# Kernel tuning notes

Hardware: AMD Instinct MI355X
Metric: run time of the kernel (lower is better)

## Reference

```python
import jax, jax.numpy as jnp
import numpy as np
import math

MAX_L = 3
N_RBF = 8
CUTOFF = 5.5
P_CUT = 6
ZS = (1, 6, 7, 8)
N_NODES = 10000
N_EDGES = 60000
N_EMB = 3  # n_atom_basis; edge channels = N_EMB**2 = 9


def _lxlylz_list(max_l):
    lst = []
    for l in range(max_l + 1):
        for lx in range(l, -1, -1):
            for ly in range(l - lx, -1, -1):
                lst.append((lx, ly, l - lx - ly))
    return lst

LXLYLZ = _lxlylz_list(MAX_L)            # 20 monomial exponent triples
IDX = {v: i for i, v in enumerate(LXLYLZ)}
L_OF = np.array([sum(v) for v in LXLYLZ], dtype=np.int32)
LX = jnp.array([v[0] for v in LXLYLZ])
LY = jnp.array([v[1] for v in LXLYLZ])
LZ = jnp.array([v[2] for v in LXLYLZ])
L_OF_J = jnp.array(L_OF)
ZS_J = jnp.array(ZS)


def _multinom(v):
    l = sum(v)
    return math.factorial(l) // (math.factorial(v[0]) * math.factorial(v[1]) * math.factorial(v[2]))


def _splits(l):
    return [v for v in LXLYLZ if sum(v) == l]


def _nu2_terms():
    # B2_l = sum_{|lvec|=l} multinom(lvec) * A_lvec^2  (contraction of (r1.r2)^l)
    out = []
    for l in range(1, MAX_L + 1):
        vs = _splits(l)
        idx = jnp.array([IDX[v] for v in vs])
        pref = jnp.array([float(_multinom(v)) for v in vs], dtype=jnp.float32)
        out.append((idx, idx, pref))
    return out


def _nu3_terms():
    # invariants from (r1.r2)^e12 (r1.r3)^e13 (r2.r3)^e23, all e>=1, vector degrees <= MAX_L
    combos = [(a, b, c) for a in range(1, MAX_L + 1) for b in range(1, MAX_L + 1)
              for c in range(1, MAX_L + 1) if a + b <= MAX_L and a + c <= MAX_L and b + c <= MAX_L]
    out = []
    for (e12, e13, e23) in combos:
        coef = {}
        for va in _splits(e12):
            for vb in _splits(e13):
                for vc in _splits(e23):
                    v1 = (va[0] + vb[0], va[1] + vb[1], va[2] + vb[2])
                    v2 = (va[0] + vc[0], va[1] + vc[1], va[2] + vc[2])
                    v3 = (vb[0] + vc[0], vb[1] + vc[1], vb[2] + vc[2])
                    key = (v1, v2, v3)
                    coef[key] = coef.get(key, 0.0) + float(_multinom(va) * _multinom(vb) * _multinom(vc))
        keys = list(coef.keys())
        i1 = jnp.array([IDX[k[0]] for k in keys])
        i2 = jnp.array([IDX[k[1]] for k in keys])
        i3 = jnp.array([IDX[k[2]] for k in keys])
        pref = jnp.array([coef[k] for k in keys], dtype=jnp.float32)
        out.append((i1, i2, i3, pref))
    return out

NU2_TERMS = _nu2_terms()
NU3_TERMS = _nu3_terms()


def setup_inputs() -> dict:
    key = jax.random.key(0)
    k1, k2, k3, k4, k5 = jax.random.split(key, 5)
    positions = jax.random.uniform(k1, (N_NODES, 3), dtype=jnp.float32) * 4.0  # box so most r < cutoff
    atomic_numbers = ZS_J[jax.random.randint(k2, (N_NODES,), 0, len(ZS))]
    edge_index = jax.random.randint(k3, (2, N_EDGES), 0, N_NODES)
    shifts = jnp.zeros((N_EDGES, 3), jnp.float32)
    embedding_weight = jax.random.normal(k4, (len(ZS), N_EMB), jnp.float32) / np.sqrt(len(ZS))
    radial_weight = jax.random.normal(k5, (MAX_L + 1, N_RBF, N_RBF), jnp.float32) / np.sqrt(N_RBF)
    return {"positions": positions, "shifts": shifts, "embedding_weight": embedding_weight,
            "radial_weight": radial_weight, "atomic_numbers": atomic_numbers, "edge_index": edge_index}


def reference(positions, shifts, embedding_weight, radial_weight, atomic_numbers, edge_index):
    # node one-hot + embedding
    onehot = (atomic_numbers[:, None] == ZS_J[None, :]).astype(positions.dtype)
    emb = onehot @ embedding_weight                                   # [N, n_emb]
    snd, rcv = edge_index[0], edge_index[1]
    E = snd.shape[0]
    # directed edge encoding: outer product of endpoint embeddings -> [E, n_emb^2]
    enc = (emb[snd][:, :, None] * emb[rcv][:, None, :]).reshape(E, -1)
    # edge vectors / lengths (normalized)
    vec = positions[rcv] - positions[snd] + shifts
    length = jnp.maximum(jnp.linalg.norm(vec, axis=-1, keepdims=True), 1e-9)  # [E,1]
    unit = vec / length
    # Bessel RBF * polynomial cutoff
    n = jnp.arange(1, N_RBF + 1, dtype=positions.dtype)
    rbf = jnp.sqrt(2.0 / CUTOFF) * jnp.sin(n * jnp.pi * length / CUTOFF) / length  # [E,R]
    x = length / CUTOFF
    p = float(P_CUT)
    fc = (1.0 - 0.5 * (p + 1) * (p + 2) * x ** P_CUT + p * (p + 2) * x ** (P_CUT + 1)
          - 0.5 * p * (p + 1) * x ** (P_CUT + 2)) * (x < 1.0)
    radial = rbf * fc                                                  # [E,R]
    # angular monomials x^lx y^ly z^lz
    pw = unit[:, :, None] ** jnp.arange(MAX_L + 1)                     # [E,3,L+1]
    ang = pw[:, 0, LX] * pw[:, 1, LY] * pw[:, 2, LZ]                   # [E,A=20]
    # triple outer product -> per-edge attribute tensor [E,R,A,C]
    edge_attr = jnp.einsum('er,ea,ec->erac', radial, ang, enc)
    # shared per-l radial linear transform
    Wa = radial_weight[L_OF_J]                                         # [A,R,R]
    edge_attr = jnp.einsum('ars,erac->esac', Wa, edge_attr)
    # scatter-sum to receiver nodes -> A basis
    A = jax.ops.segment_sum(edge_attr, rcv, num_segments=positions.shape[0])  # [N,R,A,C]
    # symmetrizer: invariant B basis up to nu=3
    feats = [A[:, :, 0, :]]                                            # nu=1: A_{000}
    for i1, i2, pref in NU2_TERMS:
        feats.append(jnp.einsum('t,nrtc->nrc', pref, A[:, :, i1, :] * A[:, :, i2, :]))
    for i1, i2, i3, pref in NU3_TERMS:
        feats.append(jnp.einsum('t,nrtc->nrc', pref, A[:, :, i1, :] * A[:, :, i2, :] * A[:, :, i3, :]))
    return jnp.stack(feats, axis=2)                                    # [N, R, n_B=8, C]
```

## Files before the change

kernel.cpp:

```cpp
#include <hip/hip_runtime.h>

constexpr int NRBF = 8;
constexpr int NA   = 20;
constexpr int NC   = 9;
constexpr int EDW  = 64;
constexpr int CAP  = 64;
constexpr int STG  = 16;

__constant__ int cLX[NA] = {0,1,0,0,2,1,1,0,0,0,3,2,2,1,1,1,0,0,0,0};
__constant__ int cLY[NA] = {0,0,1,0,0,1,0,2,1,0,0,1,0,2,1,0,3,2,1,0};
__constant__ int cLZ[NA] = {0,0,0,1,0,0,1,0,1,2,0,0,1,0,1,2,0,1,2,3};
__constant__ int cLOF[NA]= {0,1,1,1,2,2,2,2,2,2,3,3,3,3,3,3,3,3,3,3};
constexpr int kLOF[NA]  = {0,1,1,1,2,2,2,2,2,2,3,3,3,3,3,3,3,3,3,3};

__device__ __forceinline__ int zmap(int z) {
    return z == 1 ? 0 : (z == 6 ? 1 : (z == 7 ? 2 : 3));
}

struct Nu3Tbl {
    int n;
    unsigned char i1[200], i2[200], i3[200], cb[200];
    float pref[200];
};
constexpr int idx_of(int lx, int ly, int lz) {
    int l = lx + ly + lz;
    int base = (l == 0) ? 0 : ((l == 1) ? 1 : ((l == 2) ? 4 : 10));
    int d = l - lx;
    return base + d * (d + 1) / 2 + (d - ly);
}
constexpr int factc(int k) { return k <= 1 ? 1 : k * factc(k - 1); }
constexpr float multinom(int lx, int ly, int lz) {
    return (float)(factc(lx + ly + lz) / (factc(lx) * factc(ly) * factc(lz)));
}
constexpr Nu3Tbl make_nu3() {
    Nu3Tbl t{};
    const int combos[4][3] = {{1,1,1},{1,1,2},{1,2,1},{2,1,1}};
    for (int q = 0; q < 4; ++q) {
        int e12 = combos[q][0], e13 = combos[q][1], e23 = combos[q][2];
        for (int ax = e12; ax >= 0; --ax) for (int ay = e12-ax; ay >= 0; --ay) { int az = e12-ax-ay;
        for (int bx = e13; bx >= 0; --bx) for (int by = e13-bx; by >= 0; --by) { int bz = e13-bx-by;
        for (int cx = e23; cx >= 0; --cx) for (int cy = e23-cx; cy >= 0; --cy) { int cz = e23-cx-cy;
            t.i1[t.n] = (unsigned char)idx_of(ax+bx, ay+by, az+bz);
            t.i2[t.n] = (unsigned char)idx_of(ax+cx, ay+cy, az+cz);
            t.i3[t.n] = (unsigned char)idx_of(bx+cx, by+cy, bz+cz);
            t.cb[t.n] = (unsigned char)q;
            t.pref[t.n] = multinom(ax,ay,az) * multinom(bx,by,bz) * multinom(cx,cy,cz);
            t.n++;
        }}}
    }
    return t;
}
constexpr Nu3Tbl NU3 = make_nu3();

__global__ __launch_bounds__(256) void precompute_kernel(
    const float* __restrict__ pos, const float* __restrict__ shifts,
    const float* __restrict__ embW, const float* __restrict__ radW,
    const int* __restrict__ zs, const int* __restrict__ eidx,
    float* __restrict__ edata, int* __restrict__ counts, int* __restrict__ order,
    int E)
{
    __shared__ float s_rad[4][NRBF];
    int w = threadIdx.x >> 6;
    int lane = threadIdx.x & 63;
    int e = blockIdx.x * 4 + w;
    bool valid = (e < E);

    int snd = 0, rcv = 0;
    float dx = 0.f, dy = 0.f, dz = 0.f, len = 1.f;
    if (valid) {
        snd = eidx[e]; rcv = eidx[E + e];
        dx = pos[rcv*3+0] - pos[snd*3+0] + shifts[e*3+0];
        dy = pos[rcv*3+1] - pos[snd*3+1] + shifts[e*3+1];
        dz = pos[rcv*3+2] - pos[snd*3+2] + shifts[e*3+2];
        len = fmaxf(sqrtf(dx*dx + dy*dy + dz*dz), 1e-9f);
    }
    if (valid && lane < 8) {
        float x = len * (1.0f / 5.5f);
        float fc = 0.f;
        if (x < 1.f) {
            float x2 = x * x, x6 = x2 * x2 * x2;
            fc = 1.f - 28.f * x6 + 48.f * x6 * x - 21.f * x6 * x2;
        }
        float rbf = 0.60302268915552724f *
                    sinf((float)(lane + 1) * 3.14159265358979323846f * len / 5.5f) / len;
        s_rad[w][lane] = rbf * fc;
    }
    __syncthreads();
    if (valid) {
        float v = 0.f;
        if (lane < 32) {
            int l = lane >> 3, s = lane & 7;
            float acc = 0.f;
            #pragma unroll
            for (int r = 0; r < 8; ++r) acc += radW[(l * 8 + r) * 8 + s] * s_rad[w][r];
            v = acc;
        } else if (lane < 52) {
            int a = lane - 32;
            float inv = 1.f / len;
            float ux = dx * inv, uy = dy * inv, uz = dz * inv;
            float t = 1.f;
            for (int k = 0; k < cLX[a]; ++k) t *= ux;
            for (int k = 0; k < cLY[a]; ++k) t *= uy;
            for (int k = 0; k < cLZ[a]; ++k) t *= uz;
            v = t;
        } else if (lane < 61) {
            int t = lane - 52;
            v = embW[zmap(zs[snd]) * 3 + t / 3] * embW[zmap(zs[rcv]) * 3 + t % 3];
        }
        edata[(size_t)e * EDW + lane] = v;
        if (lane == 0) {
            int p = atomicAdd(&counts[rcv], 1);
            if (p < CAP) order[rcv * CAP + p] = e;
        }
    }
}

__global__ __launch_bounds__(128) void node_kernel(
    const float* __restrict__ edata, const int* __restrict__ counts,
    const int* __restrict__ order, float* __restrict__ out, int N)
{
    int n = blockIdx.x;
    if (n >= N) return;
    __shared__ float ed[STG][EDW];
    __shared__ int   sidx[STG];
    __shared__ float Bsh[NRBF * 8 * NC];
    int tid = threadIdx.x;
    int deg = min(counts[n], CAP);

    bool active = (tid < NRBF * NC);
    int s_i = tid / NC, c_i = tid % NC;

    float Av[NA];
    #pragma unroll
    for (int a = 0; a < NA; ++a) Av[a] = 0.f;

    for (int base = 0; base < deg; base += STG) {
        int nb = min(STG, deg - base);
        if (tid < nb) sidx[tid] = order[n * CAP + base + tid];
        __syncthreads();
        for (int i = tid; i < nb * EDW; i += 128)
            ed[i >> 6][i & 63] = edata[(size_t)sidx[i >> 6] * EDW + (i & 63)];
        __syncthreads();
        if (active) {
            for (int m = 0; m < nb; ++m) {
                float ec = ed[m][52 + c_i];
                float rl[4];
                rl[0] = ed[m][ 0 + s_i] * ec;
                rl[1] = ed[m][ 8 + s_i] * ec;
                rl[2] = ed[m][16 + s_i] * ec;
                rl[3] = ed[m][24 + s_i] * ec;
                #pragma unroll
                for (int a = 0; a < NA; ++a)
                    Av[a] += rl[kLOF[a]] * ed[m][32 + a];
            }
        }
        __syncthreads();
    }

    if (active) {
        float b0 = Av[0];
        float b1 = Av[1]*Av[1] + Av[2]*Av[2] + Av[3]*Av[3];
        float b2 = Av[4]*Av[4] + 2.f*Av[5]*Av[5] + 2.f*Av[6]*Av[6]
                 + Av[7]*Av[7] + 2.f*Av[8]*Av[8] + Av[9]*Av[9];
        float b3 = Av[10]*Av[10] + 3.f*(Av[11]*Av[11] + Av[12]*Av[12] + Av[13]*Av[13])
                 + 6.f*Av[14]*Av[14] + 3.f*Av[15]*Av[15] + Av[16]*Av[16]
                 + 3.f*(Av[17]*Av[17] + Av[18]*Av[18]) + Av[19]*Av[19];
        float b4 = 0.f, b5 = 0.f, b6 = 0.f, b7 = 0.f;
        #pragma unroll
        for (int k = 0; k < NU3.n; ++k) {
            float term = NU3.pref[k] * Av[NU3.i1[k]] * Av[NU3.i2[k]] * Av[NU3.i3[k]];
            if      (NU3.cb[k] == 0) b4 += term;
            else if (NU3.cb[k] == 1) b5 += term;
            else if (NU3.cb[k] == 2) b6 += term;
            else                     b7 += term;
        }
        int sb = s_i * 8 * NC + c_i;
        Bsh[sb + 0*NC] = b0; Bsh[sb + 1*NC] = b1; Bsh[sb + 2*NC] = b2; Bsh[sb + 3*NC] = b3;
        Bsh[sb + 4*NC] = b4; Bsh[sb + 5*NC] = b5; Bsh[sb + 6*NC] = b6; Bsh[sb + 7*NC] = b7;
    }
    __syncthreads();
    float* op = out + (size_t)n * (NRBF * 8 * NC);
    for (int i = tid; i < NRBF * 8 * NC; i += 128) op[i] = Bsh[i];
}

extern "C" void kernel_launch(void* const* d_in, const int* in_sizes, int n_in,
                              void* d_out, int out_size, void* d_ws, size_t ws_size,
                              hipStream_t stream) {
    const float* pos    = (const float*)d_in[0];
    const float* shifts = (const float*)d_in[1];
    const float* embW   = (const float*)d_in[2];
    const float* radW   = (const float*)d_in[3];
    const int*   zs     = (const int*)d_in[4];
    const int*   eidx   = (const int*)d_in[5];
    float* out = (float*)d_out;

    int N = in_sizes[0] / 3;
    int E = in_sizes[5] / 2;

    float* edata = (float*)d_ws;
    int* counts  = (int*)(edata + (size_t)E * EDW);
    int* order   = counts + N;

    hipMemsetAsync(counts, 0, (size_t)N * sizeof(int), stream);

    precompute_kernel<<<dim3((E + 3) / 4), dim3(256), 0, stream>>>(
        pos, shifts, embW, radW, zs, eidx, edata, counts, order, E);

    node_kernel<<<dim3(N), dim3(128), 0, stream>>>(edata, counts, order, out, N);
}
```

Measured before the change: 129.2 us.

## Use warp shuffles for radial basis, float4 edge staging, larger stage size

The precompute kernel drops its shared-memory staging and block barrier, broadcasting the eight radial values with wavefront shuffles and returning early for out-of-range edges. The node kernel gathers edge records with float4 loads instead of scalar loads and stages 24 edges per pass instead of 16. It also skips the trailing barrier on the last pass. This cuts load instruction count and synchronisation, at the cost of somewhat more shared memory per block.

Result: no change. 131.6 us (+1.9%).

```diff
diff --git a/kernel.cpp b/kernel.cpp
--- a/kernel.cpp
+++ b/kernel.cpp
@@ -5,12 +5,11 @@
 constexpr int NC   = 9;
 constexpr int EDW  = 64;
 constexpr int CAP  = 64;
-constexpr int STG  = 16;
+constexpr int STG  = 24;
 
 __constant__ int cLX[NA] = {0,1,0,0,2,1,1,0,0,0,3,2,2,1,1,1,0,0,0,0};
 __constant__ int cLY[NA] = {0,0,1,0,0,1,0,2,1,0,0,1,0,2,1,0,3,2,1,0};
 __constant__ int cLZ[NA] = {0,0,0,1,0,0,1,0,1,2,0,0,1,0,1,2,0,1,2,3};
-__constant__ int cLOF[NA]= {0,1,1,1,2,2,2,2,2,2,3,3,3,3,3,3,3,3,3,3};
 constexpr int kLOF[NA]  = {0,1,1,1,2,2,2,2,2,2,3,3,3,3,3,3,3,3,3,3};
 
 __device__ __forceinline__ int zmap(int z) {
@@ -59,22 +58,19 @@
     float* __restrict__ edata, int* __restrict__ counts, int* __restrict__ order,
     int E)
 {
-    __shared__ float s_rad[4][NRBF];
     int w = threadIdx.x >> 6;
     int lane = threadIdx.x & 63;
     int e = blockIdx.x * 4 + w;
-    bool valid = (e < E);
-
-    int snd = 0, rcv = 0;
-    float dx = 0.f, dy = 0.f, dz = 0.f, len = 1.f;
-    if (valid) {
-        snd = eidx[e]; rcv = eidx[E + e];
-        dx = pos[rcv*3+0] - pos[snd*3+0] + shifts[e*3+0];
-        dy = pos[rcv*3+1] - pos[snd*3+1] + shifts[e*3+1];
-        dz = pos[rcv*3+2] - pos[snd*3+2] + shifts[e*3+2];
-        len = fmaxf(sqrtf(dx*dx + dy*dy + dz*dz), 1e-9f);
-    }
-    if (valid && lane < 8) {
+    if (e >= E) return;
+
+    int snd = eidx[e], rcv = eidx[E + e];
+    float dx = pos[rcv*3+0] - pos[snd*3+0] + shifts[e*3+0];
+    float dy = pos[rcv*3+1] - pos[snd*3+1] + shifts[e*3+1];
+    float dz = pos[rcv*3+2] - pos[snd*3+2] + shifts[e*3+2];
+    float len = fmaxf(sqrtf(dx*dx + dy*dy + dz*dz), 1e-9f);
+
+    float myrad = 0.f;
+    if (lane < 8) {
         float x = len * (1.0f / 5.5f);
         float fc = 0.f;
         if (x < 1.f) {
@@ -83,35 +79,34 @@
         }
         float rbf = 0.60302268915552724f *
                     sinf((float)(lane + 1) * 3.14159265358979323846f * len / 5.5f) / len;
-        s_rad[w][lane] = rbf * fc;
-    }
-    __syncthreads();
-    if (valid) {
-        float v = 0.f;
-        if (lane < 32) {
-            int l = lane >> 3, s = lane & 7;
-            float acc = 0.f;
-            #pragma unroll
-            for (int r = 0; r < 8; ++r) acc += radW[(l * 8 + r) * 8 + s] * s_rad[w][r];
-            v = acc;
-        } else if (lane < 52) {
-            int a = lane - 32;
-            float inv = 1.f / len;
-            float ux = dx * inv, uy = dy * inv, uz = dz * inv;
-            float t = 1.f;
-            for (int k = 0; k < cLX[a]; ++k) t *= ux;
-            for (int k = 0; k < cLY[a]; ++k) t *= uy;
-            for (int k = 0; k < cLZ[a]; ++k) t *= uz;
-            v = t;
-        } else if (lane < 61) {
-            int t = lane - 52;
-            v = embW[zmap(zs[snd]) * 3 + t / 3] * embW[zmap(zs[rcv]) * 3 + t % 3];
-        }
-        edata[(size_t)e * EDW + lane] = v;
-        if (lane == 0) {
-            int p = atomicAdd(&counts[rcv], 1);
-            if (p < CAP) order[rcv * CAP + p] = e;
-        }
+        myrad = rbf * fc;
+    }
+    float r0 = __shfl(myrad, 0), r1 = __shfl(myrad, 1), r2 = __shfl(myrad, 2),
+          r3 = __shfl(myrad, 3), r4 = __shfl(myrad, 4), r5 = __shfl(myrad, 5),
+          r6 = __shfl(myrad, 6), r7 = __shfl(myrad, 7);
+    float v = 0.f;
+    if (lane < 32) {
+        int l = lane >> 3, s = lane & 7;
+        const float* Wl = radW + l * 64 + s;
+        v = Wl[0]*r0 + Wl[8]*r1 + Wl[16]*r2 + Wl[24]*r3
+          + Wl[32]*r4 + Wl[40]*r5 + Wl[48]*r6 + Wl[56]*r7;
+    } else if (lane < 52) {
+        int a = lane - 32;
+        float inv = 1.f / len;
+        float ux = dx * inv, uy = dy * inv, uz = dz * inv;
+        float t = 1.f;
+        for (int k = 0; k < cLX[a]; ++k) t *= ux;
+        for (int k = 0; k < cLY[a]; ++k) t *= uy;
+        for (int k = 0; k < cLZ[a]; ++k) t *= uz;
+        v = t;
+    } else if (lane < 61) {
+        int t = lane - 52;
+        v = embW[zmap(zs[snd]) * 3 + t / 3] * embW[zmap(zs[rcv]) * 3 + t % 3];
+    }
+    edata[(size_t)e * EDW + lane] = v;
+    if (lane == 0) {
+        int p = atomicAdd(&counts[rcv], 1);
+        if (p < CAP) order[rcv * CAP + p] = e;
     }
 }
 
@@ -138,8 +133,12 @@
         int nb = min(STG, deg - base);
         if (tid < nb) sidx[tid] = order[n * CAP + base + tid];
         __syncthreads();
-        for (int i = tid; i < nb * EDW; i += 128)
-            ed[i >> 6][i & 63] = edata[(size_t)sidx[i >> 6] * EDW + (i & 63)];
+        for (int i = tid; i < nb * 16; i += 128) {
+            int rec = i >> 4, q = i & 15;
+            float4 v = reinterpret_cast<const float4*>(
+                           edata + (size_t)sidx[rec] * EDW)[q];
+            reinterpret_cast<float4*>(ed[rec])[q] = v;
+        }
         __syncthreads();
         if (active) {
             for (int m = 0; m < nb; ++m) {
@@ -154,7 +153,7 @@
                     Av[a] += rl[kLOF[a]] * ed[m][32 + a];
             }
         }
-        __syncthreads();
+        if (base + STG < deg) __syncthreads();
     }
 
     if (active) {
```
